# Kernel optimization log

Measured on AMD Instinct MI355X. Metric: run time of the kernel, lower is better.

The kernel has to match this reference:

```python
import jax, jax.numpy as jnp
import numpy as np

S = 896.0          # image size in pixels
T = 28             # mask resolution
ALPHA, GAMMA = 0.25, 2.0
EPS = 1e-8
CAND_K = 10        # SimOTA candidate topk
CLS_W, L1_W, GIOU_W, MASK_W = 2.0, 5.0, 2.0, 5.0
CENTER_R = 0.05 * S  # center-region radius (approximates mmdet 2.5*stride)


def _areas(b):
    return jnp.clip(b[..., 2] - b[..., 0], 0) * jnp.clip(b[..., 3] - b[..., 1], 0)


def pairwise_iou_giou(a, b, eps=EPS):
    # a [n,4], b [m,4] xyxy -> (iou [n,m], giou [n,m])
    lt = jnp.maximum(a[:, None, :2], b[None, :, :2])
    rb = jnp.minimum(a[:, None, 2:], b[None, :, 2:])
    wh = jnp.clip(rb - lt, 0)
    inter = wh[..., 0] * wh[..., 1]
    union = _areas(a)[:, None] + _areas(b)[None, :] - inter
    iou = inter / (union + eps)
    elt = jnp.minimum(a[:, None, :2], b[None, :, :2])
    erb = jnp.maximum(a[:, None, 2:], b[None, :, 2:])
    ewh = jnp.clip(erb - elt, 0)
    enc = ewh[..., 0] * ewh[..., 1]
    return iou, iou - (enc - union) / (enc + eps)


def elementwise_giou(a, b, eps=EPS):
    # a,b [n,4] matched pairs -> giou [n] (the diag of generalized_box_iou)
    lt = jnp.maximum(a[:, :2], b[:, :2]); rb = jnp.minimum(a[:, 2:], b[:, 2:])
    wh = jnp.clip(rb - lt, 0); inter = wh[:, 0] * wh[:, 1]
    union = _areas(a) + _areas(b) - inter
    iou = inter / (union + eps)
    elt = jnp.minimum(a[:, :2], b[:, :2]); erb = jnp.maximum(a[:, 2:], b[:, 2:])
    ewh = jnp.clip(erb - elt, 0); enc = ewh[:, 0] * ewh[:, 1]
    return iou - (enc - union) / (enc + eps)


def crop_resize(img, box, scale, t=T):
    # img [C,H,W]; box [4] xyxy in image pixels; scale: pixels -> grid units.
    C, H, W = img.shape
    x1, y1, x2, y2 = box * scale
    xs = x1 + (x2 - x1) * (jnp.arange(t, dtype=img.dtype) + 0.5) / t - 0.5
    ys = y1 + (y2 - y1) * (jnp.arange(t, dtype=img.dtype) + 0.5) / t - 0.5
    X = jnp.broadcast_to(xs[None, :], (t, t))
    Y = jnp.broadcast_to(ys[:, None], (t, t))
    x0f = jnp.clip(jnp.floor(X), 0, W - 1); y0f = jnp.clip(jnp.floor(Y), 0, H - 1)
    wx = jnp.clip(X - x0f, 0, 1); wy = jnp.clip(Y - y0f, 0, 1)
    x0 = x0f.astype(jnp.int32); y0 = y0f.astype(jnp.int32)
    x1i = jnp.clip(x0 + 1, 0, W - 1); y1i = jnp.clip(y0 + 1, 0, H - 1)
    g = lambda yi, xi: img[:, yi, xi]  # [C,t,t]
    return (g(y0, x0) * (1 - wx) * (1 - wy) + g(y0, x1i) * wx * (1 - wy)
            + g(y1i, x0) * (1 - wx) * wy + g(y1i, x1i) * wx * wy)


def match_image(logits, boxes, gt_cls, gt_box):
    # SimOTA matcher (no-grad). logits [n,c], boxes [n,4] xyxy, gt_cls [m], gt_box [m,4]
    n, c = logits.shape
    m = gt_cls.shape[0]
    cx = (boxes[:, 0] + boxes[:, 2]) * 0.5
    cy = (boxes[:, 1] + boxes[:, 3]) * 0.5
    in_gt = ((cx[:, None] >= gt_box[None, :, 0]) & (cx[:, None] <= gt_box[None, :, 2])
             & (cy[:, None] >= gt_box[None, :, 1]) & (cy[:, None] <= gt_box[None, :, 3]))
    gcx = (gt_box[:, 0] + gt_box[:, 2]) * 0.5
    gcy = (gt_box[:, 1] + gt_box[:, 3]) * 0.5
    in_ct = ((jnp.abs(cx[:, None] - gcx[None, :]) <= CENTER_R)
             & (jnp.abs(cy[:, None] - gcy[None, :]) <= CENTER_R))
    valid = jnp.any(in_gt | in_ct, axis=1)              # [n]
    in_both = in_gt & in_ct                             # [n,m]
    # FocalLossCost (mmdet): pos - neg at gt class
    p = jax.nn.sigmoid(logits)
    neg = -jnp.log(1 - p + EPS) * (1 - ALPHA) * p ** GAMMA
    pos = -jnp.log(p + EPS) * ALPHA * (1 - p) ** GAMMA
    cls_cost = CLS_W * (pos - neg)[:, gt_cls]           # [n,m]
    nb = boxes / S; ngb = gt_box / S
    l1_cost = L1_W * jnp.sum(jnp.abs(nb[:, None, :] - ngb[None, :, :]), axis=-1)
    iou, _ = pairwise_iou_giou(boxes, gt_box)
    _, ngiou = pairwise_iou_giou(nb, ngb)
    cost = (cls_cost + l1_cost + GIOU_W * (1 - ngiou)
            + jnp.where(in_both, 0.0, 1e5) + jnp.where(valid[:, None], 0.0, 1e9))
    # dynamic-k assignment
    ious_v = jnp.where(valid[:, None], iou, 0.0)
    topk_ious, _ = jax.lax.top_k(ious_v.T, CAND_K)      # [m,CAND_K]
    dyn_k = jnp.clip(jnp.sum(topk_ious, axis=1).astype(jnp.int32), 1, n)
    ranks = jnp.argsort(jnp.argsort(cost, axis=0), axis=0)
    matching = (ranks < dyn_k[None, :]) & valid[:, None]
    best = jnp.argmin(cost, axis=1)
    multi = jnp.sum(matching, axis=1) > 1
    one_hot_best = jnp.arange(m)[None, :] == best[:, None]
    matching = jnp.where(multi[:, None], one_hot_best, matching)
    assigned = jnp.any(matching, axis=1)
    gt_ind = jnp.where(assigned, jnp.argmax(matching, axis=1), best)
    return valid, gt_ind


def image_loss(logits, boxes, feat, w_mask, gt_cls, gt_box, gt_mask):
    n, c = logits.shape
    sg = jax.lax.stop_gradient
    valid, gt_ind = match_image(sg(logits), sg(boxes), gt_cls, sg(gt_box))
    w = valid.astype(logits.dtype)
    mcls = gt_cls[gt_ind]                               # [n]
    mbox = gt_box[gt_ind]                               # [n,4]
    # sigmoid focal loss over all proposals; invalid ones get all-zero labels
    labels = (jnp.arange(c)[None, :] == mcls[:, None]).astype(logits.dtype) * w[:, None]
    p = jax.nn.sigmoid(logits)
    ce = jnp.logaddexp(0.0, logits) - logits * labels   # BCE-with-logits, stable
    p_t = p * labels + (1 - p) * (1 - labels)
    a_t = ALPHA * labels + (1 - ALPHA) * (1 - labels)
    cls_loss = jnp.sum(a_t * (1 - p_t) ** GAMMA * ce)
    nb = boxes / S; ngb = mbox / S
    l1_loss = jnp.sum(jnp.abs(nb - ngb) * w[:, None])
    giou_loss = jnp.sum((1 - elementwise_giou(nb, ngb)) * w)
    # mask head: ROI bilinear crop + per-class linear projection
    feat_scale = feat.shape[-1] / S
    crop = jax.vmap(lambda bx: crop_resize(feat, bx, feat_scale))(boxes)  # [n,Cf,T,T]
    wsel = w_mask[mcls]                                 # [n,Cf]
    m_pred = jax.nn.sigmoid(jnp.einsum('nfyx,nf->nyx', crop, wsel)).reshape(n, -1)
    mask_scale = gt_mask.shape[-1] / S
    gcrop = jax.vmap(lambda msk, bx: crop_resize(msk[None], bx, mask_scale)[0])(
        gt_mask[gt_ind], mbox).reshape(n, -1)
    inter = jnp.sum(m_pred * gcrop, axis=-1)
    union = jnp.sum(m_pred, axis=-1) + jnp.sum(gcrop, axis=-1) + EPS
    mask_loss = jnp.sum((1 - 2 * inter / union) * w)
    return cls_loss, l1_loss, giou_loss, mask_loss, jnp.sum(w)


def _make_boxes(key, shape, min_sz, max_sz):
    k1, k2 = jax.random.split(key)
    ctr = jax.random.uniform(k1, shape + (2,), minval=0.15 * S, maxval=0.85 * S)
    wh = jax.random.uniform(k2, shape + (2,), minval=min_sz, maxval=max_sz)
    return jnp.concatenate([jnp.clip(ctr - wh / 2, 0, S), jnp.clip(ctr + wh / 2, 0, S)], axis=-1)


def setup_inputs() -> dict:
    key = jax.random.key(0)
    ks = jax.random.split(key, 8)
    b, n, c, m, cf, hf, hm = 4, 300, 80, 24, 128, 64, 224
    return {
        'pred_logits': jax.random.normal(ks[0], (b, n, c), jnp.float32),
        'pred_boxes': _make_boxes(ks[1], (b, n), 20.0, 200.0),
        'features': jax.random.normal(ks[2], (b, cf, hf, hf), jnp.float32),
        'w_mask': jax.random.normal(ks[3], (c, cf), jnp.float32) * 0.05,
        'gt_classes': jax.random.randint(ks[4], (b, m), 0, c),
        'gt_boxes': _make_boxes(ks[5], (b, m), 80.0, 400.0),
        'gt_masks': (jax.random.uniform(ks[6], (b, m, hm, hm)) > 0.5).astype(jnp.float32),
    }


def reference(pred_logits, pred_boxes, features, w_mask, gt_classes, gt_boxes, gt_masks):
    per = jax.vmap(image_loss, in_axes=(0, 0, 0, None, 0, 0, 0))(
        pred_logits, pred_boxes, features, w_mask, gt_classes, gt_boxes, gt_masks)
    cls_l, l1_l, giou_l, mask_l, ninst = (jnp.sum(x) for x in per)
    # single diffusion stage (len(outputs) == 1)
    return jnp.stack([CLS_W * cls_l / ninst, L1_W * l1_l / ninst,
                      GIOU_W * giou_l / ninst, MASK_W * mask_l / ninst])
```

## Files before the change

### kernel.cpp

```cpp
#include <hip/hip_runtime.h>
#include <math.h>

#define N_PROP 300
#define N_CLS  80
#define N_GT   24
#define N_B    4
#define CF     128
#define HF     64
#define HM     224
#define TT     28
#define ALPHA  0.25f
#define EPSV   1e-8f
#define CAND_K 10
#define CENTER_R 44.8f
#define S_IMG 896.0f


__device__ __forceinline__ float iou_unnorm(const float* a, const float* g) {
    float lx = fmaxf(a[0], g[0]), ly = fmaxf(a[1], g[1]);
    float rx = fminf(a[2], g[2]), ry = fminf(a[3], g[3]);
    float w = fmaxf(rx - lx, 0.f), h = fmaxf(ry - ly, 0.f);
    float inter = w * h;
    float aa = fmaxf(a[2] - a[0], 0.f) * fmaxf(a[3] - a[1], 0.f);
    float ag = fmaxf(g[2] - g[0], 0.f) * fmaxf(g[3] - g[1], 0.f);
    float uni = aa + ag - inter;
    return inter / (uni + EPSV);
}

__device__ __forceinline__ float giou_pair(const float* a, const float* g) {
    float lx = fmaxf(a[0], g[0]), ly = fmaxf(a[1], g[1]);
    float rx = fminf(a[2], g[2]), ry = fminf(a[3], g[3]);
    float w = fmaxf(rx - lx, 0.f), h = fmaxf(ry - ly, 0.f);
    float inter = w * h;
    float aa = fmaxf(a[2] - a[0], 0.f) * fmaxf(a[3] - a[1], 0.f);
    float ag = fmaxf(g[2] - g[0], 0.f) * fmaxf(g[3] - g[1], 0.f);
    float uni = aa + ag - inter;
    float iou = inter / (uni + EPSV);
    float elx = fminf(a[0], g[0]), ely = fminf(a[1], g[1]);
    float erx = fmaxf(a[2], g[2]), ery = fmaxf(a[3], g[3]);
    float ew = fmaxf(erx - elx, 0.f), eh = fmaxf(ery - ely, 0.f);
    float enc = ew * eh;
    return iou - (enc - uni) / (enc + EPSV);
}

__device__ __forceinline__ float bilin(const float* img, int H, int W, float X, float Y) {
    float x0f = fminf(fmaxf(floorf(X), 0.f), (float)(W - 1));
    float y0f = fminf(fmaxf(floorf(Y), 0.f), (float)(H - 1));
    float wx = fminf(fmaxf(X - x0f, 0.f), 1.f);
    float wy = fminf(fmaxf(Y - y0f, 0.f), 1.f);
    int x0 = (int)x0f, y0 = (int)y0f;
    int x1 = min(x0 + 1, W - 1), y1 = min(y0 + 1, H - 1);
    float v00 = img[y0 * W + x0], v01 = img[y0 * W + x1];
    float v10 = img[y1 * W + x0], v11 = img[y1 * W + x1];
    return v00 * (1.f - wx) * (1.f - wy) + v01 * wx * (1.f - wy)
         + v10 * (1.f - wx) * wy + v11 * wx * wy;
}

__device__ __forceinline__ float focal_term(float x, float label) {
    float p = 1.f / (1.f + expf(-x));
    float ce = fmaxf(x, 0.f) + log1pf(expf(-fabsf(x))) - x * label;
    float pt = p * label + (1.f - p) * (1.f - label);
    float at = ALPHA * label + (1.f - ALPHA) * (1.f - label);
    return at * (1.f - pt) * (1.f - pt) * ce;
}

__global__ __launch_bounds__(256) void prep_kernel(
    const float* __restrict__ feat, const float* __restrict__ wm,
    const int* __restrict__ gtcls, const float* __restrict__ gtbox,
    const float* __restrict__ gmask, float* __restrict__ proj,
    float* __restrict__ gcrop, float* __restrict__ gsum)
{
    int blk = blockIdx.x;
    int tid = threadIdx.x;

    __shared__ __align__(16) float s_w[CF][N_GT];
    __shared__ float s_acc[4][64][N_GT + 1];
    __shared__ float s_rs[4];

    if (blk < 256) {
        int b = blk >> 6;
        int chunk = blk & 63;
        for (int k = tid; k < N_GT * CF; k += 256) {
            int j = k >> 7, f = k & 127;
            s_w[f][j] = wm[gtcls[b * N_GT + j] * CF + f];
        }
        __syncthreads();

        int px = tid & 63;
        int fq = tid >> 6;
        int pix = chunk * 64 + px;
        const float* fb = feat + ((size_t)b * CF + fq * 32) * (HF * HF) + pix;
        float accv[N_GT];
        #pragma unroll
        for (int j = 0; j < N_GT; j++) accv[j] = 0.f;
        #pragma unroll 8
        for (int f = 0; f < 32; f++) {
            float v = fb[(size_t)f * HF * HF];
            const float4* wrow = (const float4*)&s_w[fq * 32 + f][0];
            #pragma unroll
            for (int q = 0; q < 6; q++) {
                float4 wv = wrow[q];
                accv[q * 4 + 0] = fmaf(wv.x, v, accv[q * 4 + 0]);
                accv[q * 4 + 1] = fmaf(wv.y, v, accv[q * 4 + 1]);
                accv[q * 4 + 2] = fmaf(wv.z, v, accv[q * 4 + 2]);
                accv[q * 4 + 3] = fmaf(wv.w, v, accv[q * 4 + 3]);
            }
        }
        #pragma unroll
        for (int j = 0; j < N_GT; j++) s_acc[fq][px][j] = accv[j];
        __syncthreads();
        for (int o = tid; o < 64 * N_GT; o += 256) {
            int j = o >> 6, p2 = o & 63;
            float s = s_acc[0][p2][j] + s_acc[1][p2][j] + s_acc[2][p2][j] + s_acc[3][p2][j];
            proj[(size_t)(b * N_GT + j) * (HF * HF) + chunk * 64 + p2] = s;
        }
    } else {
        int bj = blk - 256;
        int b = bj / N_GT;
        int j = bj - b * N_GT;
        const float* gimg = gmask + (size_t)(b * N_GT + j) * HM * HM;
        float4 g4 = ((const float4*)gtbox)[b * N_GT + j];
        const float ms = 224.0f / 896.0f;
        float gx1 = g4.x * ms, gy1 = g4.y * ms, gx2 = g4.z * ms, gy2 = g4.w * ms;
        float sg = 0.f;
        #pragma unroll 4
        for (int t = tid; t < TT * TT; t += 256) {
            int ty = t / TT, tx = t - ty * TT;
            float qx = ((float)tx + 0.5f) / (float)TT;
            float qy = ((float)ty + 0.5f) / (float)TT;
            float Xg = gx1 + (gx2 - gx1) * qx - 0.5f;
            float Yg = gy1 + (gy2 - gy1) * qy - 0.5f;
            float gc = bilin(gimg, HM, HM, Xg, Yg);
            gcrop[(size_t)bj * (TT * TT) + t] = gc;
            sg += gc;
        }
        #pragma unroll
        for (int off = 32; off > 0; off >>= 1) sg += __shfl_xor(sg, off);
        if ((tid & 63) == 0) s_rs[tid >> 6] = sg;
        __syncthreads();
        if (tid == 0) gsum[bj] = ((s_rs[0] + s_rs[1]) + s_rs[2]) + s_rs[3];
    }
}

__global__ __launch_bounds__(320) void colmatch_kernel(
    const float* __restrict__ logits, const float* __restrict__ boxes,
    const int* __restrict__ gtcls, const float* __restrict__ gtbox,
    float* __restrict__ costT, unsigned int* __restrict__ matchcol)
{
    int bj = blockIdx.x;
    int b = bj / N_GT;
    int j = bj - b * N_GT;
    int tid = threadIdx.x;
    __shared__ float s_cost[N_PROP];
    __shared__ float s_iou[N_PROP];
    __shared__ float s_gball[N_GT][4];
    __shared__ int s_valid[N_PROP];
    __shared__ unsigned int s_match[10];

    if (tid < N_GT * 4) ((float*)s_gball)[tid] = gtbox[b * N_GT * 4 + tid];
    if (tid < 10) s_match[tid] = 0u;
    __syncthreads();

    int cls_j = gtcls[b * N_GT + j];
    if (tid < N_PROP) {
        int p = tid;
        const float* ap = boxes + (b * N_PROP + p) * 4;
        float a[4] = {ap[0], ap[1], ap[2], ap[3]};
        float cx = (a[0] + a[2]) * 0.5f;
        float cy = (a[1] + a[3]) * 0.5f;
        int any = 0, inb_j = 0;
        for (int q = 0; q < N_GT; q++) {
            const float* g = s_gball[q];
            int in_gt = (cx >= g[0]) & (cx <= g[2]) & (cy >= g[1]) & (cy <= g[3]);
            float gcx = (g[0] + g[2]) * 0.5f;
            float gcy = (g[1] + g[3]) * 0.5f;
            int in_ct = (fabsf(cx - gcx) <= CENTER_R) & (fabsf(cy - gcy) <= CENTER_R);
            any |= in_gt | in_ct;
            if (q == j) inb_j = in_gt & in_ct;
        }
        s_valid[p] = any;
        const float* g = s_gball[j];
        float x = logits[(size_t)(b * N_PROP + p) * N_CLS + cls_j];
        float pr = 1.f / (1.f + expf(-x));
        float neg = (-logf(1.f - pr + EPSV)) * (1.f - ALPHA) * (pr * pr);
        float pos = (-logf(pr + EPSV)) * ALPHA * ((1.f - pr) * (1.f - pr));
        float clsc = 2.0f * (pos - neg);
        float nb[4], ng[4];
        for (int k = 0; k < 4; k++) { nb[k] = a[k] / S_IMG; ng[k] = g[k] / S_IMG; }
        float l1 = 5.0f * (((fabsf(nb[0] - ng[0]) + fabsf(nb[1] - ng[1]))
                            + fabsf(nb[2] - ng[2])) + fabsf(nb[3] - ng[3]));
        float ngiou = giou_pair(nb, ng);
        float cst = clsc + l1;
        cst = cst + 2.0f * (1.f - ngiou);
        cst = cst + (inb_j ? 0.f : 1e5f);
        cst = cst + (any ? 0.f : 1e9f);
        s_cost[p] = cst;
        costT[(size_t)(b * N_PROP + p) * N_GT + j] = cst;
        s_iou[p] = any ? iou_unnorm(a, s_gball[j]) : 0.f;
    }
    __syncthreads();

    if (tid < 64) {
        int lane = tid;
        float iv[5]; int ii[5];
        #pragma unroll
        for (int c = 0; c < 5; c++) {
            int idx = c * 64 + lane;
            iv[c] = (idx < N_PROP) ? s_iou[idx] : -1.f;
            ii[c] = idx;
        }
        float ksum = 0.f;
        #pragma unroll
        for (int t = 0; t < CAND_K; t++) {
            float bv = iv[0]; int bi = ii[0];
            #pragma unroll
            for (int c = 1; c < 5; c++)
                if (iv[c] > bv || (iv[c] == bv && ii[c] < bi)) { bv = iv[c]; bi = ii[c]; }
            #pragma unroll
            for (int off = 1; off < 64; off <<= 1) {
                float ov = __shfl_xor(bv, off);
                int oi = __shfl_xor(bi, off);
                if (ov > bv || (ov == bv && oi < bi)) { bv = ov; bi = oi; }
            }
            ksum += bv;
            #pragma unroll
            for (int c = 0; c < 5; c++) if (ii[c] == bi) iv[c] = -1.f;
        }
        int dynk = max(1, min((int)ksum, N_PROP));

        float cv[5]; int ci[5];
        #pragma unroll
        for (int c = 0; c < 5; c++) {
            int idx = c * 64 + lane;
            cv[c] = (idx < N_PROP) ? s_cost[idx] : 3e38f;
            ci[c] = idx;
        }
        for (int t = 0; t < dynk; t++) {
            float bv = cv[0]; int bi = ci[0];
            #pragma unroll
            for (int c = 1; c < 5; c++)
                if (cv[c] < bv || (cv[c] == bv && ci[c] < bi)) { bv = cv[c]; bi = ci[c]; }
            #pragma unroll
            for (int off = 1; off < 64; off <<= 1) {
                float ov = __shfl_xor(bv, off);
                int oi = __shfl_xor(bi, off);
                if (ov < bv || (ov == bv && oi < bi)) { bv = ov; bi = oi; }
            }
            if (lane == 0 && s_valid[bi])
                s_match[bi >> 5] |= 1u << (bi & 31);
            #pragma unroll
            for (int c = 0; c < 5; c++) if (ci[c] == bi) cv[c] = 3e38f;
        }
    }
    __syncthreads();
    if (tid < 10) matchcol[bj * 10 + tid] = s_match[tid];
}

__global__ __launch_bounds__(256) void final_kernel(
    const float* __restrict__ logits, const float* __restrict__ boxes,
    const int* __restrict__ gtcls, const float* __restrict__ gtbox,
    const float* __restrict__ costT, const unsigned int* __restrict__ matchcol,
    const float* __restrict__ proj, const float* __restrict__ gcrop,
    const float* __restrict__ gsum, float* __restrict__ part)
{
    int e = blockIdx.x;
    int b = e / N_PROP;
    int i = e - b * N_PROP;
    int tid = threadIdx.x;

    __shared__ int s_gi, s_any;
    __shared__ float s_l1, s_gl;
    __shared__ float4 s_red[4];
    __shared__ float s_pmap[HF * HF];
    __shared__ float s_gc[TT * TT];

    if (tid < 64) {
        int lane = tid;
        float4 a4 = ((const float4*)boxes)[e];
        int ql = (lane < N_GT) ? lane : 0;
        float4 g4 = ((const float4*)gtbox)[b * N_GT + ql];

        float cx = (a4.x + a4.z) * 0.5f;
        float cy = (a4.y + a4.w) * 0.5f;
        int vb = 0;
        if (lane < N_GT) {
            int in_gt = (cx >= g4.x) & (cx <= g4.z) & (cy >= g4.y) & (cy <= g4.w);
            float gcx = (g4.x + g4.z) * 0.5f;
            float gcy = (g4.y + g4.w) * 0.5f;
            int in_ct = (fabsf(cx - gcx) <= CENTER_R) & (fabsf(cy - gcy) <= CENTER_R);
            vb = in_gt | in_ct;
        }
        int any = (__ballot(vb) != 0ULL);
        float w = any ? 1.f : 0.f;

        float cv = 3e38f;
        int idx = 63;
        if (lane < N_GT) { cv = costT[(size_t)e * N_GT + lane]; idx = lane; }
        #pragma unroll
        for (int off = 1; off < 64; off <<= 1) {
            float oc = __shfl_xor(cv, off);
            int oi = __shfl_xor(idx, off);
            if (oc < cv || (oc == cv && oi < idx)) { cv = oc; idx = oi; }
        }
        int best = idx;

        int bit = 0;
        if (lane < N_GT)
            bit = (int)((matchcol[(b * N_GT + lane) * 10 + (i >> 5)] >> (i & 31)) & 1u);
        unsigned long long bm = __ballot(bit);
        int msk = (int)(bm & 0xFFFFFFULL);
        if (__popc(msk) > 1) msk = 1 << best;
        int gi = msk ? (__ffs(msk) - 1) : best;

        float gx = __shfl(g4.x, gi), gy = __shfl(g4.y, gi);
        float gz = __shfl(g4.z, gi), gw = __shfl(g4.w, gi);

        float l1 = 0.f, gl = 0.f;
        if (any) {
            float nb[4] = {a4.x / S_IMG, a4.y / S_IMG, a4.z / S_IMG, a4.w / S_IMG};
            float ng[4] = {gx / S_IMG, gy / S_IMG, gz / S_IMG, gw / S_IMG};
            l1 = (((fabsf(nb[0] - ng[0]) + fabsf(nb[1] - ng[1]))
                   + fabsf(nb[2] - ng[2])) + fabsf(nb[3] - ng[3]));
            gl = 1.f - giou_pair(nb, ng);
        }
        if (lane == 0) {
            s_gi = gi; s_any = any; s_l1 = l1; s_gl = gl;
        }
    }
    __syncthreads();

    int gi = s_gi;
    int any = s_any;
    float w = any ? 1.f : 0.f;

    if (any) {
        const float* pimg = proj + (size_t)(b * N_GT + gi) * (HF * HF);
        const float* gcr = gcrop + (size_t)(b * N_GT + gi) * (TT * TT);
        for (int k = tid; k < HF * HF; k += 256) s_pmap[k] = pimg[k];
        for (int k = tid; k < TT * TT; k += 256) s_gc[k] = gcr[k];
    }

    int mc = gtcls[b * N_GT + gi];
    float clsv = 0.f;
    if (tid < N_CLS)
        clsv = focal_term(logits[(size_t)e * N_CLS + tid], (tid == mc) ? w : 0.f);
    __syncthreads();

    float inter = 0.f, sp = 0.f;
    if (any) {
        float4 a4 = ((const float4*)boxes)[e];
        const float fs = 64.0f / 896.0f;
        float px1 = a4.x * fs, py1 = a4.y * fs, px2 = a4.z * fs, py2 = a4.w * fs;
        #pragma unroll 4
        for (int t = tid; t < TT * TT; t += 256) {
            int ty = t / TT, tx = t - ty * TT;
            float qx = ((float)tx + 0.5f) / (float)TT;
            float qy = ((float)ty + 0.5f) / (float)TT;
            float X = px1 + (px2 - px1) * qx - 0.5f;
            float Y = py1 + (py2 - py1) * qy - 0.5f;
            float lg = bilin(s_pmap, HF, HF, X, Y);
            float mp = 1.f / (1.f + expf(-lg));
            inter += mp * s_gc[t];
            sp += mp;
        }
    }

    #pragma unroll
    for (int off = 32; off > 0; off >>= 1) {
        clsv  += __shfl_xor(clsv, off);
        inter += __shfl_xor(inter, off);
        sp    += __shfl_xor(sp, off);
    }
    if ((tid & 63) == 0) s_red[tid >> 6] = make_float4(clsv, inter, sp, 0.f);
    __syncthreads();
    if (tid == 0) {
        float4 t = s_red[0];
        for (int k = 1; k < 4; k++) {
            t.x += s_red[k].x; t.y += s_red[k].y; t.z += s_red[k].z;
        }
        float sg = any ? gsum[b * N_GT + gi] : 0.f;
        float mterm = any ? (1.f - 2.f * t.y / (t.z + sg + EPSV)) * w : 0.f;
        float* pp = part + (size_t)e * 8;
        *(float4*)pp = make_float4(t.x, any ? s_l1 : 0.f, any ? s_gl : 0.f, mterm);
        pp[4] = w;
    }
}

__global__ __launch_bounds__(256) void fin_kernel(
    const float* __restrict__ part, float* __restrict__ out)
{
    int tid = threadIdx.x;
    __shared__ float s_red[4][5];
    float s0 = 0.f, s1 = 0.f, s2 = 0.f, s3 = 0.f, s4 = 0.f;
    for (int p = tid; p < N_B * N_PROP; p += 256) {
        const float* pp = part + (size_t)p * 8;
        float4 v = *(const float4*)pp;
        s0 += v.x; s1 += v.y; s2 += v.z; s3 += v.w; s4 += pp[4];
    }
    #pragma unroll
    for (int off = 32; off > 0; off >>= 1) {
        s0 += __shfl_xor(s0, off);
        s1 += __shfl_xor(s1, off);
        s2 += __shfl_xor(s2, off);
        s3 += __shfl_xor(s3, off);
        s4 += __shfl_xor(s4, off);
    }
    if ((tid & 63) == 0) {
        int wv = tid >> 6;
        s_red[wv][0] = s0; s_red[wv][1] = s1; s_red[wv][2] = s2;
        s_red[wv][3] = s3; s_red[wv][4] = s4;
    }
    __syncthreads();
    if (tid == 0) {
        float t0 = 0.f, t1 = 0.f, t2 = 0.f, t3 = 0.f, t4 = 0.f;
        for (int k = 0; k < 4; k++) {
            t0 += s_red[k][0]; t1 += s_red[k][1]; t2 += s_red[k][2];
            t3 += s_red[k][3]; t4 += s_red[k][4];
        }
        out[0] = 2.0f * t0 / t4;
        out[1] = 5.0f * t1 / t4;
        out[2] = 2.0f * t2 / t4;
        out[3] = 5.0f * t3 / t4;
    }
}


extern "C" void kernel_launch(void* const* d_in, const int* in_sizes, int n_in,
                              void* d_out, int out_size, void* d_ws, size_t ws_size,
                              hipStream_t stream)
{
    const float* logits = (const float*)d_in[0];
    const float* boxes  = (const float*)d_in[1];
    const float* feat   = (const float*)d_in[2];
    const float* wm     = (const float*)d_in[3];
    const int*   gtcls  = (const int*)d_in[4];
    const float* gtbox  = (const float*)d_in[5];
    const float* gmask  = (const float*)d_in[6];
    float* out = (float*)d_out;
    float* ws  = (float*)d_ws;

    float* costT = ws;
    unsigned int* matchcol = (unsigned int*)(ws + 28800);
    float* part  = ws + 28800 + 960;
    float* proj  = ws + 28800 + 960 + 9600;
    float* gcrop = proj + 393216;
    float* gsum  = gcrop + 75264;

    hipLaunchKernelGGL(prep_kernel, dim3(256 + N_B * N_GT), dim3(256), 0, stream,
                       feat, wm, gtcls, gtbox, gmask, proj, gcrop, gsum);
    hipLaunchKernelGGL(colmatch_kernel, dim3(N_B * N_GT), dim3(320), 0, stream,
                       logits, boxes, gtcls, gtbox, costT, matchcol);
    hipLaunchKernelGGL(final_kernel, dim3(N_B * N_PROP), dim3(256), 0, stream,
                       logits, boxes, gtcls, gtbox, costT, matchcol, proj, gcrop, gsum, part);
    hipLaunchKernelGGL(fin_kernel, dim3(1), dim3(256), 0, stream, part, out);
}
```

Before: 117.4 us.

## Fuse final reduction into last block and read mask maps directly from global

Removes the separate single-block reduction kernel: each final_kernel block increments a global counter, and the last block to finish sums the per-proposal partials and writes the output. The counter is reset inside prep_kernel. The final kernel also stops staging the 64x64 projected map and the 28x28 ground-truth crop in shared memory and samples them straight from global/L2, which saves a 16 KB copy and a barrier per block. Cost matching is now skipped for proposals with no valid ground truth. In exchange it relies on cached global gathers and on threadfence/atomic ordering for the last-block pattern.

```diff
diff --git a/kernel.cpp b/kernel.cpp
--- a/kernel.cpp
+++ b/kernel.cpp
@@ -68,10 +68,11 @@
     const float* __restrict__ feat, const float* __restrict__ wm,
     const int* __restrict__ gtcls, const float* __restrict__ gtbox,
     const float* __restrict__ gmask, float* __restrict__ proj,
-    float* __restrict__ gcrop, float* __restrict__ gsum)
+    float* __restrict__ gcrop, float* __restrict__ gsum, int* __restrict__ cnt)
 {
     int blk = blockIdx.x;
     int tid = threadIdx.x;
+    if (blk == 0 && tid == 0) *cnt = 0;
 
     __shared__ __align__(16) float s_w[CF][N_GT];
     __shared__ float s_acc[4][64][N_GT + 1];
@@ -261,7 +262,8 @@
     const int* __restrict__ gtcls, const float* __restrict__ gtbox,
     const float* __restrict__ costT, const unsigned int* __restrict__ matchcol,
     const float* __restrict__ proj, const float* __restrict__ gcrop,
-    const float* __restrict__ gsum, float* __restrict__ part)
+    const float* __restrict__ gsum, float* __restrict__ part,
+    int* __restrict__ cnt, float* __restrict__ out)
 {
     int e = blockIdx.x;
     int b = e / N_PROP;
@@ -271,8 +273,8 @@
     __shared__ int s_gi, s_any;
     __shared__ float s_l1, s_gl;
     __shared__ float4 s_red[4];
-    __shared__ float s_pmap[HF * HF];
-    __shared__ float s_gc[TT * TT];
+    __shared__ int s_last;
+    __shared__ float s_fin[4][5];
 
     if (tid < 64) {
         int lane = tid;
@@ -291,32 +293,31 @@
             vb = in_gt | in_ct;
         }
         int any = (__ballot(vb) != 0ULL);
-        float w = any ? 1.f : 0.f;
-
-        float cv = 3e38f;
-        int idx = 63;
-        if (lane < N_GT) { cv = costT[(size_t)e * N_GT + lane]; idx = lane; }
-        #pragma unroll
-        for (int off = 1; off < 64; off <<= 1) {
-            float oc = __shfl_xor(cv, off);
-            int oi = __shfl_xor(idx, off);
-            if (oc < cv || (oc == cv && oi < idx)) { cv = oc; idx = oi; }
-        }
-        int best = idx;
-
-        int bit = 0;
-        if (lane < N_GT)
-            bit = (int)((matchcol[(b * N_GT + lane) * 10 + (i >> 5)] >> (i & 31)) & 1u);
-        unsigned long long bm = __ballot(bit);
-        int msk = (int)(bm & 0xFFFFFFULL);
-        if (__popc(msk) > 1) msk = 1 << best;
-        int gi = msk ? (__ffs(msk) - 1) : best;
-
-        float gx = __shfl(g4.x, gi), gy = __shfl(g4.y, gi);
-        float gz = __shfl(g4.z, gi), gw = __shfl(g4.w, gi);
-
+
+        int gi = 0;
         float l1 = 0.f, gl = 0.f;
         if (any) {
+            float cv = 3e38f;
+            int idx = 63;
+            if (lane < N_GT) { cv = costT[(size_t)e * N_GT + lane]; idx = lane; }
+            #pragma unroll
+            for (int off = 1; off < 64; off <<= 1) {
+                float oc = __shfl_xor(cv, off);
+                int oi = __shfl_xor(idx, off);
+                if (oc < cv || (oc == cv && oi < idx)) { cv = oc; idx = oi; }
+            }
+            int best = idx;
+
+            int bit = 0;
+            if (lane < N_GT)
+                bit = (int)((matchcol[(b * N_GT + lane) * 10 + (i >> 5)] >> (i & 31)) & 1u);
+            unsigned long long bm = __ballot(bit);
+            int msk = (int)(bm & 0xFFFFFFULL);
+            if (__popc(msk) > 1) msk = 1 << best;
+            gi = msk ? (__ffs(msk) - 1) : best;
+
+            float gx = __shfl(g4.x, gi), gy = __shfl(g4.y, gi);
+            float gz = __shfl(g4.z, gi), gw = __shfl(g4.w, gi);
             float nb[4] = {a4.x / S_IMG, a4.y / S_IMG, a4.z / S_IMG, a4.w / S_IMG};
             float ng[4] = {gx / S_IMG, gy / S_IMG, gz / S_IMG, gw / S_IMG};
             l1 = (((fabsf(nb[0] - ng[0]) + fabsf(nb[1] - ng[1]))
@@ -333,22 +334,16 @@
     int any = s_any;
     float w = any ? 1.f : 0.f;
 
-    if (any) {
-        const float* pimg = proj + (size_t)(b * N_GT + gi) * (HF * HF);
-        const float* gcr = gcrop + (size_t)(b * N_GT + gi) * (TT * TT);
-        for (int k = tid; k < HF * HF; k += 256) s_pmap[k] = pimg[k];
-        for (int k = tid; k < TT * TT; k += 256) s_gc[k] = gcr[k];
-    }
-
     int mc = gtcls[b * N_GT + gi];
     float clsv = 0.f;
     if (tid < N_CLS)
         clsv = focal_term(logits[(size_t)e * N_CLS + tid], (tid == mc) ? w : 0.f);
-    __syncthreads();
 
     float inter = 0.f, sp = 0.f;
     if (any) {
         float4 a4 = ((const float4*)boxes)[e];
+        const float* pimg = proj + (size_t)(b * N_GT + gi) * (HF * HF);
+        const float* gcr = gcrop + (size_t)(b * N_GT + gi) * (TT * TT);
         const float fs = 64.0f / 896.0f;
         float px1 = a4.x * fs, py1 = a4.y * fs, px2 = a4.z * fs, py2 = a4.w * fs;
         #pragma unroll 4
@@ -358,9 +353,9 @@
             float qy = ((float)ty + 0.5f) / (float)TT;
             float X = px1 + (px2 - px1) * qx - 0.5f;
             float Y = py1 + (py2 - py1) * qy - 0.5f;
-            float lg = bilin(s_pmap, HF, HF, X, Y);
+            float lg = bilin(pimg, HF, HF, X, Y);
             float mp = 1.f / (1.f + expf(-lg));
-            inter += mp * s_gc[t];
+            inter += mp * gcr[t];
             sp += mp;
         }
     }
@@ -384,43 +379,46 @@
         *(float4*)pp = make_float4(t.x, any ? s_l1 : 0.f, any ? s_gl : 0.f, mterm);
         pp[4] = w;
     }
-}
-
-__global__ __launch_bounds__(256) void fin_kernel(
-    const float* __restrict__ part, float* __restrict__ out)
-{
-    int tid = threadIdx.x;
-    __shared__ float s_red[4][5];
-    float s0 = 0.f, s1 = 0.f, s2 = 0.f, s3 = 0.f, s4 = 0.f;
-    for (int p = tid; p < N_B * N_PROP; p += 256) {
-        const float* pp = part + (size_t)p * 8;
-        float4 v = *(const float4*)pp;
-        s0 += v.x; s1 += v.y; s2 += v.z; s3 += v.w; s4 += pp[4];
-    }
-    #pragma unroll
-    for (int off = 32; off > 0; off >>= 1) {
-        s0 += __shfl_xor(s0, off);
-        s1 += __shfl_xor(s1, off);
-        s2 += __shfl_xor(s2, off);
-        s3 += __shfl_xor(s3, off);
-        s4 += __shfl_xor(s4, off);
-    }
-    if ((tid & 63) == 0) {
-        int wv = tid >> 6;
-        s_red[wv][0] = s0; s_red[wv][1] = s1; s_red[wv][2] = s2;
-        s_red[wv][3] = s3; s_red[wv][4] = s4;
-    }
-    __syncthreads();
+
+    __threadfence();
     if (tid == 0) {
-        float t0 = 0.f, t1 = 0.f, t2 = 0.f, t3 = 0.f, t4 = 0.f;
-        for (int k = 0; k < 4; k++) {
-            t0 += s_red[k][0]; t1 += s_red[k][1]; t2 += s_red[k][2];
-            t3 += s_red[k][3]; t4 += s_red[k][4];
-        }
-        out[0] = 2.0f * t0 / t4;
-        out[1] = 5.0f * t1 / t4;
-        out[2] = 2.0f * t2 / t4;
-        out[3] = 5.0f * t3 / t4;
+        int old = atomicAdd(cnt, 1);
+        s_last = (old == N_B * N_PROP - 1);
+    }
+    __syncthreads();
+    if (s_last) {
+        __threadfence();
+        float s0 = 0.f, s1 = 0.f, s2 = 0.f, s3 = 0.f, s4 = 0.f;
+        for (int p = tid; p < N_B * N_PROP; p += 256) {
+            const float* pp = part + (size_t)p * 8;
+            float4 v = *(const float4*)pp;
+            s0 += v.x; s1 += v.y; s2 += v.z; s3 += v.w; s4 += pp[4];
+        }
+        #pragma unroll
+        for (int off = 32; off > 0; off >>= 1) {
+            s0 += __shfl_xor(s0, off);
+            s1 += __shfl_xor(s1, off);
+            s2 += __shfl_xor(s2, off);
+            s3 += __shfl_xor(s3, off);
+            s4 += __shfl_xor(s4, off);
+        }
+        if ((tid & 63) == 0) {
+            int wv = tid >> 6;
+            s_fin[wv][0] = s0; s_fin[wv][1] = s1; s_fin[wv][2] = s2;
+            s_fin[wv][3] = s3; s_fin[wv][4] = s4;
+        }
+        __syncthreads();
+        if (tid == 0) {
+            float t0 = 0.f, t1 = 0.f, t2 = 0.f, t3 = 0.f, t4 = 0.f;
+            for (int k = 0; k < 4; k++) {
+                t0 += s_fin[k][0]; t1 += s_fin[k][1]; t2 += s_fin[k][2];
+                t3 += s_fin[k][3]; t4 += s_fin[k][4];
+            }
+            out[0] = 2.0f * t0 / t4;
+            out[1] = 5.0f * t1 / t4;
+            out[2] = 2.0f * t2 / t4;
+            out[3] = 5.0f * t3 / t4;
+        }
     }
 }
 
@@ -445,12 +443,13 @@
     float* proj  = ws + 28800 + 960 + 9600;
     float* gcrop = proj + 393216;
     float* gsum  = gcrop + 75264;
+    int*   cnt   = (int*)(gsum + 96);
 
     hipLaunchKernelGGL(prep_kernel, dim3(256 + N_B * N_GT), dim3(256), 0, stream,
-                       feat, wm, gtcls, gtbox, gmask, proj, gcrop, gsum);
+                       feat, wm, gtcls, gtbox, gmask, proj, gcrop, gsum, cnt);
     hipLaunchKernelGGL(colmatch_kernel, dim3(N_B * N_GT), dim3(320), 0, stream,
                        logits, boxes, gtcls, gtbox, costT, matchcol);
     hipLaunchKernelGGL(final_kernel, dim3(N_B * N_PROP), dim3(256), 0, stream,
-                       logits, boxes, gtcls, gtbox, costT, matchcol, proj, gcrop, gsum, part);
-    hipLaunchKernelGGL(fin_kernel, dim3(1), dim3(256), 0, stream, part, out);
-}
+                       logits, boxes, gtcls, gtbox, costT, matchcol, proj, gcrop,
+                       gsum, part, cnt, out);
+}
```

Result: slower. 200.4 us (+70.7%).

## Fuse column matching into prep kernel and read mask maps directly from global

Applied to the files above, without the earlier changes.

The SimOTA column-matching kernel is merged into the prep kernel as an extra 96 blocks, which removes one launch and lets matching run alongside the projection and crop work. In the final kernel, the per-proposal copy of the 64x64 projected map and the ground-truth crop into shared memory is dropped, along with a barrier; bilinear sampling now reads straight from global/L2. The cost argmin and match lookup are also skipped for proposals with no valid candidate. The trade-offs are scattered global reads in the sampling loop and a prep kernel that carries more shared memory per block, which may lower occupancy.

```diff
diff --git a/kernel.cpp b/kernel.cpp
--- a/kernel.cpp
+++ b/kernel.cpp
@@ -66,15 +66,22 @@
 
 __global__ __launch_bounds__(256) void prep_kernel(
     const float* __restrict__ feat, const float* __restrict__ wm,
+    const float* __restrict__ logits, const float* __restrict__ boxes,
     const int* __restrict__ gtcls, const float* __restrict__ gtbox,
     const float* __restrict__ gmask, float* __restrict__ proj,
-    float* __restrict__ gcrop, float* __restrict__ gsum)
+    float* __restrict__ gcrop, float* __restrict__ gsum,
+    float* __restrict__ costT, unsigned int* __restrict__ matchcol)
 {
     int blk = blockIdx.x;
     int tid = threadIdx.x;
 
     __shared__ __align__(16) float s_w[CF][N_GT];
     __shared__ float s_acc[4][64][N_GT + 1];
+    __shared__ float s_cost[N_PROP];
+    __shared__ float s_iou[N_PROP];
+    __shared__ float s_gball[N_GT][4];
+    __shared__ int s_valid[N_PROP];
+    __shared__ unsigned int s_match[10];
     __shared__ float s_rs[4];
 
     if (blk < 256) {
@@ -114,7 +121,7 @@
             float s = s_acc[0][p2][j] + s_acc[1][p2][j] + s_acc[2][p2][j] + s_acc[3][p2][j];
             proj[(size_t)(b * N_GT + j) * (HF * HF) + chunk * 64 + p2] = s;
         }
-    } else {
+    } else if (blk < 352) {
         int bj = blk - 256;
         int b = bj / N_GT;
         int j = bj - b * N_GT;
@@ -139,121 +146,108 @@
         if ((tid & 63) == 0) s_rs[tid >> 6] = sg;
         __syncthreads();
         if (tid == 0) gsum[bj] = ((s_rs[0] + s_rs[1]) + s_rs[2]) + s_rs[3];
-    }
-}
-
-__global__ __launch_bounds__(320) void colmatch_kernel(
-    const float* __restrict__ logits, const float* __restrict__ boxes,
-    const int* __restrict__ gtcls, const float* __restrict__ gtbox,
-    float* __restrict__ costT, unsigned int* __restrict__ matchcol)
-{
-    int bj = blockIdx.x;
-    int b = bj / N_GT;
-    int j = bj - b * N_GT;
-    int tid = threadIdx.x;
-    __shared__ float s_cost[N_PROP];
-    __shared__ float s_iou[N_PROP];
-    __shared__ float s_gball[N_GT][4];
-    __shared__ int s_valid[N_PROP];
-    __shared__ unsigned int s_match[10];
-
-    if (tid < N_GT * 4) ((float*)s_gball)[tid] = gtbox[b * N_GT * 4 + tid];
-    if (tid < 10) s_match[tid] = 0u;
-    __syncthreads();
-
-    int cls_j = gtcls[b * N_GT + j];
-    if (tid < N_PROP) {
-        int p = tid;
-        const float* ap = boxes + (b * N_PROP + p) * 4;
-        float a[4] = {ap[0], ap[1], ap[2], ap[3]};
-        float cx = (a[0] + a[2]) * 0.5f;
-        float cy = (a[1] + a[3]) * 0.5f;
-        int any = 0, inb_j = 0;
-        for (int q = 0; q < N_GT; q++) {
-            const float* g = s_gball[q];
-            int in_gt = (cx >= g[0]) & (cx <= g[2]) & (cy >= g[1]) & (cy <= g[3]);
-            float gcx = (g[0] + g[2]) * 0.5f;
-            float gcy = (g[1] + g[3]) * 0.5f;
-            int in_ct = (fabsf(cx - gcx) <= CENTER_R) & (fabsf(cy - gcy) <= CENTER_R);
-            any |= in_gt | in_ct;
-            if (q == j) inb_j = in_gt & in_ct;
-        }
-        s_valid[p] = any;
-        const float* g = s_gball[j];
-        float x = logits[(size_t)(b * N_PROP + p) * N_CLS + cls_j];
-        float pr = 1.f / (1.f + expf(-x));
-        float neg = (-logf(1.f - pr + EPSV)) * (1.f - ALPHA) * (pr * pr);
-        float pos = (-logf(pr + EPSV)) * ALPHA * ((1.f - pr) * (1.f - pr));
-        float clsc = 2.0f * (pos - neg);
-        float nb[4], ng[4];
-        for (int k = 0; k < 4; k++) { nb[k] = a[k] / S_IMG; ng[k] = g[k] / S_IMG; }
-        float l1 = 5.0f * (((fabsf(nb[0] - ng[0]) + fabsf(nb[1] - ng[1]))
-                            + fabsf(nb[2] - ng[2])) + fabsf(nb[3] - ng[3]));
-        float ngiou = giou_pair(nb, ng);
-        float cst = clsc + l1;
-        cst = cst + 2.0f * (1.f - ngiou);
-        cst = cst + (inb_j ? 0.f : 1e5f);
-        cst = cst + (any ? 0.f : 1e9f);
-        s_cost[p] = cst;
-        costT[(size_t)(b * N_PROP + p) * N_GT + j] = cst;
-        s_iou[p] = any ? iou_unnorm(a, s_gball[j]) : 0.f;
-    }
-    __syncthreads();
-
-    if (tid < 64) {
-        int lane = tid;
-        float iv[5]; int ii[5];
-        #pragma unroll
-        for (int c = 0; c < 5; c++) {
-            int idx = c * 64 + lane;
-            iv[c] = (idx < N_PROP) ? s_iou[idx] : -1.f;
-            ii[c] = idx;
-        }
-        float ksum = 0.f;
-        #pragma unroll
-        for (int t = 0; t < CAND_K; t++) {
-            float bv = iv[0]; int bi = ii[0];
+    } else {
+        int bj = blk - 352;
+        int b = bj / N_GT;
+        int j = bj - b * N_GT;
+
+        if (tid < N_GT * 4) ((float*)s_gball)[tid] = gtbox[b * N_GT * 4 + tid];
+        if (tid < 10) s_match[tid] = 0u;
+        __syncthreads();
+
+        int cls_j = gtcls[b * N_GT + j];
+        for (int p = tid; p < N_PROP; p += 256) {
+            const float* ap = boxes + (b * N_PROP + p) * 4;
+            float a[4] = {ap[0], ap[1], ap[2], ap[3]};
+            float cx = (a[0] + a[2]) * 0.5f;
+            float cy = (a[1] + a[3]) * 0.5f;
+            int any = 0, inb_j = 0;
+            for (int q = 0; q < N_GT; q++) {
+                const float* g = s_gball[q];
+                int in_gt = (cx >= g[0]) & (cx <= g[2]) & (cy >= g[1]) & (cy <= g[3]);
+                float gcx = (g[0] + g[2]) * 0.5f;
+                float gcy = (g[1] + g[3]) * 0.5f;
+                int in_ct = (fabsf(cx - gcx) <= CENTER_R) & (fabsf(cy - gcy) <= CENTER_R);
+                any |= in_gt | in_ct;
+                if (q == j) inb_j = in_gt & in_ct;
+            }
+            s_valid[p] = any;
+            const float* g = s_gball[j];
+            float x = logits[(size_t)(b * N_PROP + p) * N_CLS + cls_j];
+            float pr = 1.f / (1.f + expf(-x));
+            float neg = (-logf(1.f - pr + EPSV)) * (1.f - ALPHA) * (pr * pr);
+            float pos = (-logf(pr + EPSV)) * ALPHA * ((1.f - pr) * (1.f - pr));
+            float clsc = 2.0f * (pos - neg);
+            float nb[4], ng[4];
+            for (int k = 0; k < 4; k++) { nb[k] = a[k] / S_IMG; ng[k] = g[k] / S_IMG; }
+            float l1 = 5.0f * (((fabsf(nb[0] - ng[0]) + fabsf(nb[1] - ng[1]))
+                                + fabsf(nb[2] - ng[2])) + fabsf(nb[3] - ng[3]));
+            float ngiou = giou_pair(nb, ng);
+            float cst = clsc + l1;
+            cst = cst + 2.0f * (1.f - ngiou);
+            cst = cst + (inb_j ? 0.f : 1e5f);
+            cst = cst + (any ? 0.f : 1e9f);
+            s_cost[p] = cst;
+            costT[(size_t)(b * N_PROP + p) * N_GT + j] = cst;
+            s_iou[p] = any ? iou_unnorm(a, s_gball[j]) : 0.f;
+        }
+        __syncthreads();
+
+        if (tid < 64) {
+            int lane = tid;
+            float iv[5]; int ii[5];
             #pragma unroll
-            for (int c = 1; c < 5; c++)
-                if (iv[c] > bv || (iv[c] == bv && ii[c] < bi)) { bv = iv[c]; bi = ii[c]; }
+            for (int c = 0; c < 5; c++) {
+                int idx = c * 64 + lane;
+                iv[c] = (idx < N_PROP) ? s_iou[idx] : -1.f;
+                ii[c] = idx;
+            }
+            float ksum = 0.f;
             #pragma unroll
-            for (int off = 1; off < 64; off <<= 1) {
-                float ov = __shfl_xor(bv, off);
-                int oi = __shfl_xor(bi, off);
-                if (ov > bv || (ov == bv && oi < bi)) { bv = ov; bi = oi; }
-            }
-            ksum += bv;
+            for (int t = 0; t < CAND_K; t++) {
+                float bv = iv[0]; int bi = ii[0];
+                #pragma unroll
+                for (int c = 1; c < 5; c++)
+                    if (iv[c] > bv || (iv[c] == bv && ii[c] < bi)) { bv = iv[c]; bi = ii[c]; }
+                #pragma unroll
+                for (int off = 1; off < 64; off <<= 1) {
+                    float ov = __shfl_xor(bv, off);
+                    int oi = __shfl_xor(bi, off);
+                    if (ov > bv || (ov == bv && oi < bi)) { bv = ov; bi = oi; }
+                }
+                ksum += bv;
+                #pragma unroll
+                for (int c = 0; c < 5; c++) if (ii[c] == bi) iv[c] = -1.f;
+            }
+            int dynk = max(1, min((int)ksum, N_PROP));
+
+            float cv[5]; int ci[5];
             #pragma unroll
-            for (int c = 0; c < 5; c++) if (ii[c] == bi) iv[c] = -1.f;
-        }
-        int dynk = max(1, min((int)ksum, N_PROP));
-
-        float cv[5]; int ci[5];
-        #pragma unroll
-        for (int c = 0; c < 5; c++) {
-            int idx = c * 64 + lane;
-            cv[c] = (idx < N_PROP) ? s_cost[idx] : 3e38f;
-            ci[c] = idx;
-        }
-        for (int t = 0; t < dynk; t++) {
-            float bv = cv[0]; int bi = ci[0];
-            #pragma unroll
-            for (int c = 1; c < 5; c++)
-                if (cv[c] < bv || (cv[c] == bv && ci[c] < bi)) { bv = cv[c]; bi = ci[c]; }
-            #pragma unroll
-            for (int off = 1; off < 64; off <<= 1) {
-                float ov = __shfl_xor(bv, off);
-                int oi = __shfl_xor(bi, off);
-                if (ov < bv || (ov == bv && oi < bi)) { bv = ov; bi = oi; }
-            }
-            if (lane == 0 && s_valid[bi])
-                s_match[bi >> 5] |= 1u << (bi & 31);
-            #pragma unroll
-            for (int c = 0; c < 5; c++) if (ci[c] == bi) cv[c] = 3e38f;
-        }
-    }
-    __syncthreads();
-    if (tid < 10) matchcol[bj * 10 + tid] = s_match[tid];
+            for (int c = 0; c < 5; c++) {
+                int idx = c * 64 + lane;
+                cv[c] = (idx < N_PROP) ? s_cost[idx] : 3e38f;
+                ci[c] = idx;
+            }
+            for (int t = 0; t < dynk; t++) {
+                float bv = cv[0]; int bi = ci[0];
+                #pragma unroll
+                for (int c = 1; c < 5; c++)
+                    if (cv[c] < bv || (cv[c] == bv && ci[c] < bi)) { bv = cv[c]; bi = ci[c]; }
+                #pragma unroll
+                for (int off = 1; off < 64; off <<= 1) {
+                    float ov = __shfl_xor(bv, off);
+                    int oi = __shfl_xor(bi, off);
+                    if (ov < bv || (ov == bv && oi < bi)) { bv = ov; bi = oi; }
+                }
+                if (lane == 0 && s_valid[bi])
+                    s_match[bi >> 5] |= 1u << (bi & 31);
+                #pragma unroll
+                for (int c = 0; c < 5; c++) if (ci[c] == bi) cv[c] = 3e38f;
+            }
+        }
+        __syncthreads();
+        if (tid < 10) matchcol[bj * 10 + tid] = s_match[tid];
+    }
 }
 
 __global__ __launch_bounds__(256) void final_kernel(
@@ -271,8 +265,6 @@
     __shared__ int s_gi, s_any;
     __shared__ float s_l1, s_gl;
     __shared__ float4 s_red[4];
-    __shared__ float s_pmap[HF * HF];
-    __shared__ float s_gc[TT * TT];
 
     if (tid < 64) {
         int lane = tid;
@@ -291,32 +283,31 @@
             vb = in_gt | in_ct;
         }
         int any = (__ballot(vb) != 0ULL);
-        float w = any ? 1.f : 0.f;
-
-        float cv = 3e38f;
-        int idx = 63;
-        if (lane < N_GT) { cv = costT[(size_t)e * N_GT + lane]; idx = lane; }
-        #pragma unroll
-        for (int off = 1; off < 64; off <<= 1) {
-            float oc = __shfl_xor(cv, off);
-            int oi = __shfl_xor(idx, off);
-            if (oc < cv || (oc == cv && oi < idx)) { cv = oc; idx = oi; }
-        }
-        int best = idx;
-
-        int bit = 0;
-        if (lane < N_GT)
-            bit = (int)((matchcol[(b * N_GT + lane) * 10 + (i >> 5)] >> (i & 31)) & 1u);
-        unsigned long long bm = __ballot(bit);
-        int msk = (int)(bm & 0xFFFFFFULL);
-        if (__popc(msk) > 1) msk = 1 << best;
-        int gi = msk ? (__ffs(msk) - 1) : best;
-
-        float gx = __shfl(g4.x, gi), gy = __shfl(g4.y, gi);
-        float gz = __shfl(g4.z, gi), gw = __shfl(g4.w, gi);
-
+
+        int gi = 0;
         float l1 = 0.f, gl = 0.f;
         if (any) {
+            float cv = 3e38f;
+            int idx = 63;
+            if (lane < N_GT) { cv = costT[(size_t)e * N_GT + lane]; idx = lane; }
+            #pragma unroll
+            for (int off = 1; off < 64; off <<= 1) {
+                float oc = __shfl_xor(cv, off);
+                int oi = __shfl_xor(idx, off);
+                if (oc < cv || (oc == cv && oi < idx)) { cv = oc; idx = oi; }
+            }
+            int best = idx;
+
+            int bit = 0;
+            if (lane < N_GT)
+                bit = (int)((matchcol[(b * N_GT + lane) * 10 + (i >> 5)] >> (i & 31)) & 1u);
+            unsigned long long bm = __ballot(bit);
+            int msk = (int)(bm & 0xFFFFFFULL);
+            if (__popc(msk) > 1) msk = 1 << best;
+            gi = msk ? (__ffs(msk) - 1) : best;
+
+            float gx = __shfl(g4.x, gi), gy = __shfl(g4.y, gi);
+            float gz = __shfl(g4.z, gi), gw = __shfl(g4.w, gi);
             float nb[4] = {a4.x / S_IMG, a4.y / S_IMG, a4.z / S_IMG, a4.w / S_IMG};
             float ng[4] = {gx / S_IMG, gy / S_IMG, gz / S_IMG, gw / S_IMG};
             l1 = (((fabsf(nb[0] - ng[0]) + fabsf(nb[1] - ng[1]))
@@ -333,22 +324,16 @@
     int any = s_any;
     float w = any ? 1.f : 0.f;
 
-    if (any) {
-        const float* pimg = proj + (size_t)(b * N_GT + gi) * (HF * HF);
-        const float* gcr = gcrop + (size_t)(b * N_GT + gi) * (TT * TT);
-        for (int k = tid; k < HF * HF; k += 256) s_pmap[k] = pimg[k];
-        for (int k = tid; k < TT * TT; k += 256) s_gc[k] = gcr[k];
-    }
-
     int mc = gtcls[b * N_GT + gi];
     float clsv = 0.f;
     if (tid < N_CLS)
         clsv = focal_term(logits[(size_t)e * N_CLS + tid], (tid == mc) ? w : 0.f);
-    __syncthreads();
 
     float inter = 0.f, sp = 0.f;
     if (any) {
         float4 a4 = ((const float4*)boxes)[e];
+        const float* pimg = proj + (size_t)(b * N_GT + gi) * (HF * HF);
+        const float* gcr = gcrop + (size_t)(b * N_GT + gi) * (TT * TT);
         const float fs = 64.0f / 896.0f;
         float px1 = a4.x * fs, py1 = a4.y * fs, px2 = a4.z * fs, py2 = a4.w * fs;
         #pragma unroll 4
@@ -358,9 +343,9 @@
             float qy = ((float)ty + 0.5f) / (float)TT;
             float X = px1 + (px2 - px1) * qx - 0.5f;
             float Y = py1 + (py2 - py1) * qy - 0.5f;
-            float lg = bilin(s_pmap, HF, HF, X, Y);
+            float lg = bilin(pimg, HF, HF, X, Y);
             float mp = 1.f / (1.f + expf(-lg));
-            inter += mp * s_gc[t];
+            inter += mp * gcr[t];
             sp += mp;
         }
     }
@@ -446,11 +431,11 @@
     float* gcrop = proj + 393216;
     float* gsum  = gcrop + 75264;
 
-    hipLaunchKernelGGL(prep_kernel, dim3(256 + N_B * N_GT), dim3(256), 0, stream,
-                       feat, wm, gtcls, gtbox, gmask, proj, gcrop, gsum);
-    hipLaunchKernelGGL(colmatch_kernel, dim3(N_B * N_GT), dim3(320), 0, stream,
-                       logits, boxes, gtcls, gtbox, costT, matchcol);
+    hipLaunchKernelGGL(prep_kernel, dim3(256 + 96 + 96), dim3(256), 0, stream,
+                       feat, wm, logits, boxes, gtcls, gtbox, gmask,
+                       proj, gcrop, gsum, costT, matchcol);
     hipLaunchKernelGGL(final_kernel, dim3(N_B * N_PROP), dim3(256), 0, stream,
-                       logits, boxes, gtcls, gtbox, costT, matchcol, proj, gcrop, gsum, part);
+                       logits, boxes, gtcls, gtbox, costT, matchcol, proj, gcrop,
+                       gsum, part);
     hipLaunchKernelGGL(fin_kernel, dim3(1), dim3(256), 0, stream, part, out);
 }
```

Result: faster. 109.2 us (-7.0%).
